# Optimization experiments

Hardware: AMD Instinct MI355X
Metric: run time of the kernel (lower is better)

The kernel has to match this reference:

```python
import jax, jax.numpy as jnp
import numpy as np

B, L, H, V, P = 256, 16, 256, 5000, 4
NPG, DEG, STEPS, OUT = 150, 4, 4, 2000
N, E = B * NPG, B * NPG * DEG


def _seg_softmax(x, seg, num):
    # sparse softmax over variable-size groups (rows of the sparse matrix)
    m = jax.ops.segment_max(x, seg, num_segments=num)
    e = jnp.exp(x - m[seg])
    s = jax.ops.segment_sum(e, seg, num_segments=num)
    return e / s[seg]


def setup_inputs():
    key = jax.random.key(0)
    ks = jax.random.split(key, 24)
    questions = jax.random.normal(ks[0], (B, L, H), jnp.float32)
    lengths = jax.random.randint(ks[1], (B,), L // 2, L + 1)
    node_attrs = jax.random.normal(ks[2], (N, P - 1, H), jnp.float32)
    edge_attrs = jax.random.normal(ks[3], (E, H), jnp.float32)
    node_graph = jnp.repeat(jnp.arange(B), NPG)
    edge_graph = jnp.repeat(jnp.arange(B), NPG * DEG)
    off = jnp.repeat(jnp.arange(B) * NPG, NPG * DEG)
    edge_src = jax.random.randint(ks[4], (E,), 0, NPG) + off
    edge_dst = jax.random.randint(ks[5], (E,), 0, NPG) + off
    s = float(1.0 / np.sqrt(H))
    u = lambda k, shape: jax.random.uniform(k, shape, jnp.float32, -s, s)
    vocab = jax.random.normal(ks[6], (V, H), jnp.float32) * 0.1
    default_embed = jax.random.uniform(ks[7], (H,), jnp.float32)
    W_norm = jnp.eye(H, dtype=jnp.float32)
    lstm_Wih, lstm_Whh = u(ks[8], (4 * H, H)), u(ks[9], (4 * H, H))
    lstm_bih, lstm_bhh = u(ks[10], (4 * H,)), u(ks[11], (4 * H,))
    rnn_Wih, rnn_Whh = u(ks[12], (H, H)), u(ks[13], (H, H))
    rnn_bih, rnn_bhh = u(ks[14], (H,)), u(ks[15], (H,))
    prop_embeds = jax.random.normal(ks[16], (P, H), jnp.float32) * 0.1
    Ws_property = jax.random.uniform(ks[17], (P, H, H), jnp.float32) * s
    W_state = jax.random.uniform(ks[18], (H,), jnp.float32) * s
    W_relation = jax.random.uniform(ks[19], (H,), jnp.float32) * s
    lin_W, lin_b = u(ks[20], (OUT, 2 * H)), u(ks[21], (OUT,))
    return dict(questions=questions, node_attrs=node_attrs, edge_attrs=edge_attrs,
                vocab=vocab, default_embed=default_embed, W_norm=W_norm,
                lstm_Wih=lstm_Wih, lstm_Whh=lstm_Whh, lstm_bih=lstm_bih, lstm_bhh=lstm_bhh,
                rnn_Wih=rnn_Wih, rnn_Whh=rnn_Whh, rnn_bih=rnn_bih, rnn_bhh=rnn_bhh,
                prop_embeds=prop_embeds, Ws_property=Ws_property,
                W_state=W_state, W_relation=W_relation, lin_W=lin_W, lin_b=lin_b,
                lengths=lengths, node_graph=node_graph, edge_graph=edge_graph,
                edge_src=edge_src, edge_dst=edge_dst)


def reference(questions, node_attrs, edge_attrs, vocab, default_embed, W_norm,
              lstm_Wih, lstm_Whh, lstm_bih, lstm_bhh,
              rnn_Wih, rnn_Whh, rnn_bih, rnn_bhh,
              prop_embeds, Ws_property, W_state, W_relation, lin_W, lin_b,
              lengths, node_graph, edge_graph, edge_src, edge_dst):
    # ---- NormalizeWordsModel (tagger) ----
    words = questions.reshape(B * L, H)
    C = jnp.concatenate([vocab, default_embed[None]], axis=0)  # [V+1, H]
    Pm = jax.nn.softmax((words @ W_norm) @ C.T, axis=1)        # [B*L, V+1]
    Vtag = Pm[:, -1:] * words + Pm[:, :-1] @ vocab             # [B*L, H]
    Vpad = Vtag.reshape(B, L, H)

    # ---- LSTM encoder: final hidden at last valid step (packed-sequence semantics) ----
    valid = jnp.arange(L)[:, None] < lengths[None, :]  # [L, B]

    def lstm_step(carry, inp):
        h, c = carry
        x, v = inp
        g = x @ lstm_Wih.T + lstm_bih + h @ lstm_Whh.T + lstm_bhh
        i, f, gc, o = jnp.split(g, 4, axis=-1)  # torch gate order i,f,g,o
        c_new = jax.nn.sigmoid(f) * c + jax.nn.sigmoid(i) * jnp.tanh(gc)
        h_new = jax.nn.sigmoid(o) * jnp.tanh(c_new)
        vm = v[:, None]
        return (jnp.where(vm, h_new, h), jnp.where(vm, c_new, c)), None

    z = jnp.zeros((B, H), questions.dtype)
    (Q, _), _ = jax.lax.scan(lstm_step, (z, z), (Vpad.transpose(1, 0, 2), valid))

    # ---- InstructionsDecoder: relu RNNCell fed the same Q each step ----
    def dec_step(hx, _):
        hx = jax.nn.relu(Q @ rnn_Wih.T + rnn_bih + hx @ rnn_Whh.T + rnn_bhh)
        return hx, hx

    _, Hins = jax.lax.scan(dec_step, z, None, length=STEPS)
    Hins = Hins.transpose(1, 0, 2)  # [B, STEPS, H]

    # ---- attention over (masked) tagged words ----
    att = jnp.einsum('bnh,blh->bnl', Hins, Vpad)
    mask = jnp.arange(L)[None, None, :] < lengths[:, None, None]
    att = jnp.where(mask, att, -jnp.inf)
    R = jax.nn.softmax(att, axis=-1) @ Vpad  # instructions [B, STEPS, H]

    # ---- NSMCell recurrence ----
    nodes_per_graph = jax.ops.segment_sum(jnp.ones(N, questions.dtype), node_graph, num_segments=B)
    dist = (1.0 / nodes_per_graph)[node_graph]  # [N]
    prop_sim = None
    for step in range(STEPS):
        instr = R[:, step]  # [B, H]
        prop_sim = jax.nn.softmax(instr @ prop_embeds.T, axis=1)  # [B, P]
        transformed = jnp.einsum('phk,npk->nph', Ws_property[:-1], node_attrs)  # [N, P-1, H]
        node_scores = jax.nn.elu(jnp.sum(
            prop_sim[node_graph, :-1, None] * instr[node_graph, None, :] * transformed, axis=1))  # [N, H]
        edge_scores = jax.nn.elu(instr[edge_graph] * (edge_attrs @ Ws_property[-1].T))  # [E, H]
        p_state = _seg_softmax(node_scores @ W_state, node_graph, B)  # [N]
        agg = jax.ops.segment_sum(dist[edge_src, None] * edge_scores, edge_dst, num_segments=N)  # [N, H]
        p_rel = _seg_softmax(agg @ W_relation, node_graph, B)  # [N]
        r = prop_sim[node_graph, -1]
        dist = r * p_rel + (1.0 - r) * p_state

    # ---- readout ----
    node_feat = jnp.sum(prop_sim[node_graph, :-1, None] * node_attrs, axis=1)  # [N, H]
    aggregated = jax.ops.segment_sum(dist[:, None] * node_feat, node_graph, num_segments=B)  # [B, H]
    return jnp.concatenate([Q, aggregated], axis=1) @ lin_W.T + lin_b
```

## Files before the change

kernel.cpp:

```cpp
#include <hip/hip_runtime.h>
#include <hip/hip_bf16.h>
#include <math.h>

#define BB 256
#define LL 16
#define HH 256
#define VV 5000
#define NPG 150
#define DEG 4
#define NSTEPS 4
#define OUTD 2000
#define NN (BB*NPG)
#define EE (BB*NPG*DEG)
#define BL (BB*LL)
#define VPAD 5120
#define KPAD 5024
#define EPG (NPG*DEG)

__device__ __forceinline__ float wred_sum(float v){
  #pragma unroll
  for(int o=32;o;o>>=1) v += __shfl_down(v,o,64);
  return v;
}
__device__ __forceinline__ float wred_max(float v){
  #pragma unroll
  for(int o=32;o;o>>=1) v = fmaxf(v,__shfl_down(v,o,64));
  return v;
}
__device__ __forceinline__ float block_sum256(float v, float* sh){
  v = wred_sum(v);
  __syncthreads();
  if((threadIdx.x&63)==0) sh[threadIdx.x>>6]=v;
  __syncthreads();
  return sh[0]+sh[1]+sh[2]+sh[3];
}
__device__ __forceinline__ float block_max256(float v, float* sh){
  v = wred_max(v);
  __syncthreads();
  if((threadIdx.x&63)==0) sh[threadIdx.x>>6]=v;
  __syncthreads();
  return fmaxf(fmaxf(sh[0],sh[1]),fmaxf(sh[2],sh[3]));
}
__device__ __forceinline__ float eluf(float x){ return x>0.f ? x : expm1f(x); }
__device__ __forceinline__ float sigf(float x){ return 1.f/(1.f+expf(-x)); }
__device__ __forceinline__ float fsig(float x){
  return __builtin_amdgcn_rcpf(1.f + __expf(-x));
}
__device__ __forceinline__ float ftanh(float x){
  return 1.f - 2.f*__builtin_amdgcn_rcpf(1.f + __expf(2.f*x));
}
__device__ __forceinline__ float b2f(unsigned short s){
  union{float f; unsigned int u;} x; x.u = ((unsigned int)s)<<16; return x.f;
}
__device__ __forceinline__ unsigned short f2bf_bits(float x){
  union { __hip_bfloat16 h; unsigned short s; } u; u.h = __float2bfloat16(x); return u.s;
}

__device__ __forceinline__ void async16(void* lds, const void* g){
  __builtin_amdgcn_global_load_lds(
      (const __attribute__((address_space(1))) unsigned int*)g,
      (__attribute__((address_space(3))) unsigned int*)lds, 16, 0, 0);
}

typedef __attribute__((ext_vector_type(8))) short short8;
typedef __attribute__((ext_vector_type(4))) float f32x4;

__device__ __forceinline__ short8 pack8(float4 a, float4 b){
  short8 r;
  r[0]=(short)f2bf_bits(a.x); r[1]=(short)f2bf_bits(a.y);
  r[2]=(short)f2bf_bits(a.z); r[3]=(short)f2bf_bits(a.w);
  r[4]=(short)f2bf_bits(b.x); r[5]=(short)f2bf_bits(b.y);
  r[6]=(short)f2bf_bits(b.z); r[7]=(short)f2bf_bits(b.w);
  return r;
}

template<int EPI>
__global__ __launch_bounds__(256) void mfma_bt_bf16_k(
    const __hip_bfloat16* __restrict__ A, const __hip_bfloat16* __restrict__ Bt,
    float* __restrict__ Cf, __hip_bfloat16* __restrict__ Cb,
    int lda, int ldb, int ldc, int Nreal,
    int kItersTotal, int kPerSplit, const float* __restrict__ bias,
    const float* __restrict__ rscale)
{
  __shared__ __hip_bfloat16 As[128*32];
  __shared__ __hip_bfloat16 Bs[128*32];
  const int bm = blockIdx.y*128, bn = blockIdx.x*128;
  const int tid = threadIdx.x;
  int k0 = blockIdx.z * kPerSplit;
  int k1 = k0 + kPerSplit; if (k1 > kItersTotal) k1 = kItersTotal;
  const int lane = tid & 63, wave = tid >> 6;
  const int quad = lane >> 4, r16 = lane & 15;
  const int wr = wave >> 1, wc = wave & 1;
  f32x4 acc[4][4] = {};
  const int c0 = tid, c1 = tid + 256;
  const int ar0 = c0 >> 2, ak0 = (c0 & 3)*8;
  const int ar1 = c1 >> 2, ak1 = (c1 & 3)*8;
  const __hip_bfloat16* Ab = A + (size_t)bm*lda;
  const __hip_bfloat16* Bb = Bt + (size_t)bn*ldb;
  for (int kk = k0; kk < k1; ++kk){
    const int kb = kk*32;
    async16(&As[c0*8], Ab + (size_t)ar0*lda + kb + ak0);
    async16(&As[c1*8], Ab + (size_t)ar1*lda + kb + ak1);
    async16(&Bs[c0*8], Bb + (size_t)ar0*ldb + kb + ak0);
    async16(&Bs[c1*8], Bb + (size_t)ar1*ldb + kb + ak1);
    __syncthreads();
    short8 av[4], bv[4];
    #pragma unroll
    for (int i=0;i<4;i++){
      av[i] = *(const short8*)&As[(wr*64 + i*16 + r16)*32 + quad*8];
      bv[i] = *(const short8*)&Bs[(wc*64 + i*16 + r16)*32 + quad*8];
    }
    #pragma unroll
    for (int i=0;i<4;i++)
      #pragma unroll
      for (int j=0;j<4;j++)
        acc[i][j] = __builtin_amdgcn_mfma_f32_16x16x32_bf16(av[i], bv[j], acc[i][j], 0,0,0);
    __syncthreads();
  }
  #pragma unroll
  for (int i=0;i<4;i++){
    int row = bm + wr*64 + i*16 + quad*4;
    #pragma unroll
    for (int j=0;j<4;j++){
      int col = bn + wc*64 + j*16 + r16;
      if (col >= Nreal) continue;
      #pragma unroll
      for (int r=0;r<4;r++){
        float v = acc[i][j][r];
        if (EPI==0){ if (bias) v += bias[col]; Cf[(size_t)(row+r)*ldc + col] = v; }
        else if (EPI==1){ Cb[(size_t)(row+r)*ldc + col] = __float2bfloat16(v); }
        else { if (rscale) v *= rscale[row+r]; atomicAdd(&Cf[(size_t)(row+r)*ldc + col], v); }
      }
    }
  }
}

template<int EPI>
__global__ __launch_bounds__(256) void mfma_bt_f32_k(
    const float* __restrict__ A, const float* __restrict__ Bt,
    float* __restrict__ Cf, __hip_bfloat16* __restrict__ Cb,
    int lda, int ldb, int ldc, int Nreal,
    int kIters, const float* __restrict__ bias)
{
  __shared__ __hip_bfloat16 As[128*32];
  __shared__ __hip_bfloat16 Bs[128*32];
  const int bm = blockIdx.y*128, bn = blockIdx.x*128;
  const int tid = threadIdx.x;
  const int lane = tid & 63, wave = tid >> 6;
  const int quad = lane >> 4, r16 = lane & 15;
  const int wr = wave >> 1, wc = wave & 1;
  f32x4 acc[4][4] = {};
  for (int kk = 0; kk < kIters; ++kk){
    const int kb = kk*32;
    #pragma unroll
    for (int i=0;i<2;i++){
      int c = tid + i*256;
      int row = c >> 2, k0 = (c & 3)*8;
      const float* src = A + (size_t)(bm+row)*lda + kb + k0;
      float4 v0 = *(const float4*)(src);
      float4 v1 = *(const float4*)(src+4);
      *(short8*)&As[row*32 + k0] = pack8(v0, v1);
    }
    #pragma unroll
    for (int i=0;i<2;i++){
      int c = tid + i*256;
      int row = c >> 2, k0 = (c & 3)*8;
      float4 v0 = {0.f,0.f,0.f,0.f}, v1 = {0.f,0.f,0.f,0.f};
      if (bn + row < Nreal){
        const float* src = Bt + (size_t)(bn+row)*ldb + kb + k0;
        v0 = *(const float4*)(src);
        v1 = *(const float4*)(src+4);
      }
      *(short8*)&Bs[row*32 + k0] = pack8(v0, v1);
    }
    __syncthreads();
    short8 av[4], bv[4];
    #pragma unroll
    for (int i=0;i<4;i++){
      av[i] = *(const short8*)&As[(wr*64 + i*16 + r16)*32 + quad*8];
      bv[i] = *(const short8*)&Bs[(wc*64 + i*16 + r16)*32 + quad*8];
    }
    #pragma unroll
    for (int i=0;i<4;i++)
      #pragma unroll
      for (int j=0;j<4;j++)
        acc[i][j] = __builtin_amdgcn_mfma_f32_16x16x32_bf16(av[i], bv[j], acc[i][j], 0,0,0);
    __syncthreads();
  }
  #pragma unroll
  for (int i=0;i<4;i++){
    int row = bm + wr*64 + i*16 + quad*4;
    #pragma unroll
    for (int j=0;j<4;j++){
      int col = bn + wc*64 + j*16 + r16;
      if (col >= Nreal) continue;
      #pragma unroll
      for (int r=0;r<4;r++){
        float v = acc[i][j][r];
        if (EPI==0){ if (bias) v += bias[col]; Cf[(size_t)(row+r)*ldc + col] = v; }
        else { Cb[(size_t)(row+r)*ldc + col] = __float2bfloat16(v); }
      }
    }
  }
}

__global__ __launch_bounds__(256) void gemm_exp_k(
    const __hip_bfloat16* __restrict__ A, const __hip_bfloat16* __restrict__ Bt,
    __hip_bfloat16* __restrict__ Pm, float* __restrict__ row_sum,
    float* __restrict__ e_def)
{
  __shared__ __hip_bfloat16 As[128*32];
  __shared__ __hip_bfloat16 Bs[128*32];
  const int bm = blockIdx.y*128, bn = blockIdx.x*128;
  const int tid = threadIdx.x;
  const int lane = tid & 63, wave = tid >> 6;
  const int quad = lane >> 4, r16 = lane & 15;
  const int wr = wave >> 1, wc = wave & 1;
  f32x4 acc[4][4] = {};
  const int c0 = tid, c1 = tid + 256;
  const int ar0 = c0 >> 2, ak0 = (c0 & 3)*8;
  const int ar1 = c1 >> 2, ak1 = (c1 & 3)*8;
  const __hip_bfloat16* Ab = A + (size_t)bm*HH;
  const __hip_bfloat16* Bb = Bt + (size_t)bn*HH;
  for (int kk = 0; kk < HH/32; ++kk){
    const int kb = kk*32;
    async16(&As[c0*8], Ab + (size_t)ar0*HH + kb + ak0);
    async16(&As[c1*8], Ab + (size_t)ar1*HH + kb + ak1);
    async16(&Bs[c0*8], Bb + (size_t)ar0*HH + kb + ak0);
    async16(&Bs[c1*8], Bb + (size_t)ar1*HH + kb + ak1);
    __syncthreads();
    short8 av[4], bv[4];
    #pragma unroll
    for (int i=0;i<4;i++){
      av[i] = *(const short8*)&As[(wr*64 + i*16 + r16)*32 + quad*8];
      bv[i] = *(const short8*)&Bs[(wc*64 + i*16 + r16)*32 + quad*8];
    }
    #pragma unroll
    for (int i=0;i<4;i++)
      #pragma unroll
      for (int j=0;j<4;j++)
        acc[i][j] = __builtin_amdgcn_mfma_f32_16x16x32_bf16(av[i], bv[j], acc[i][j], 0,0,0);
    __syncthreads();
  }
  #pragma unroll
  for (int i=0;i<4;i++){
    int rowb = bm + wr*64 + i*16 + quad*4;
    float rsum[4] = {0.f,0.f,0.f,0.f};
    #pragma unroll
    for (int j=0;j<4;j++){
      int col = bn + wc*64 + j*16 + r16;
      #pragma unroll
      for (int r=0;r<4;r++){
        float e = (col <= VV) ? expf(acc[i][j][r]) : 0.f;
        rsum[r] += e;
        if (col < KPAD) Pm[(size_t)(rowb+r)*KPAD + col] = __float2bfloat16(col < VV ? e : 0.f);
        if (col == VV) e_def[rowb+r] = e;
      }
    }
    #pragma unroll
    for (int r=0;r<4;r++){
      float s = rsum[r];
      s += __shfl_xor(s, 1, 64);
      s += __shfl_xor(s, 2, 64);
      s += __shfl_xor(s, 4, 64);
      s += __shfl_xor(s, 8, 64);
      if (r16 == 0) atomicAdd(&row_sum[rowb+r], s);
    }
  }
}

__global__ __launch_bounds__(1024)
__attribute__((amdgpu_waves_per_eu(4, 4)))
void lstm_persist_k(
    const float* __restrict__ gX, const __hip_bfloat16* __restrict__ Whh_bf,
    const int* __restrict__ lengths,
    float* __restrict__ h_out, __hip_bfloat16* __restrict__ hbf_out)
{
  __shared__ __hip_bfloat16 Wl[512*132];
  __shared__ __hip_bfloat16 hbuf[2][16*264];
  const int bg = blockIdx.x, tid = threadIdx.x;
  const int lane = tid & 63, w = tid >> 6;
  const int quad = lane >> 4, r16 = lane & 15;
  const int hb = w*16;
  for (int idx = tid; idx < 512*16; idx += 1024){
    int row = idx >> 4, c8 = (idx & 15)*8;
    int ww = row >> 6, g = (row >> 4) & 3, rr = row & 15;
    *(short8*)&Wl[row*132 + c8] =
        *(const short8*)&Whh_bf[((size_t)(g*256 + ww*16 + rr))*256 + 128 + c8];
  }
  short8 rW[4][4];
  #pragma unroll
  for (int kc=0; kc<4; kc++)
    #pragma unroll
    for (int g=0; g<4; g++)
      rW[kc][g] = *(const short8*)&Whh_bf[((size_t)(g*256 + hb + r16))*256 + kc*32 + quad*8];
  for (int i = tid; i < 16*264; i += 1024) hbuf[0][i] = __float2bfloat16(0.f);
  int lenr[4];
  #pragma unroll
  for (int r=0;r<4;r++) lenr[r] = lengths[bg*16 + quad*4 + r];
  __syncthreads();
  f32x4 cstate = {0.f,0.f,0.f,0.f};
  f32x4 hstate = {0.f,0.f,0.f,0.f};
  int p = 0;
  const float* gXb = gX + (size_t)bg*16*LL*(4*HH) + hb + r16;
  for (int t=0; t<LL; t++){
    float gxv[4][4];
    #pragma unroll
    for (int r=0;r<4;r++)
      #pragma unroll
      for (int g=0;g<4;g++)
        gxv[r][g] = gXb[((size_t)((quad*4+r)*LL + t))*(4*HH) + g*HH];
    f32x4 acc[4] = {};
    const __hip_bfloat16* hr = hbuf[p];
    #pragma unroll
    for (int kc=0; kc<4; kc++){
      short8 a = *(const short8*)&hr[r16*264 + kc*32 + quad*8];
      #pragma unroll
      for (int g=0; g<4; g++)
        acc[g] = __builtin_amdgcn_mfma_f32_16x16x32_bf16(a, rW[kc][g], acc[g], 0,0,0);
    }
    if (w < 8){
      #pragma unroll
      for (int kc=4; kc<8; kc++){
        short8 a = *(const short8*)&hr[r16*264 + kc*32 + quad*8];
        #pragma unroll
        for (int g=0; g<4; g++){
          short8 b = *(const short8*)&Wl[(w*64 + g*16 + r16)*132 + (kc-4)*32 + quad*8];
          acc[g] = __builtin_amdgcn_mfma_f32_16x16x32_bf16(a, b, acc[g], 0,0,0);
        }
      }
    } else {
      #pragma unroll
      for (int kc=4; kc<8; kc++){
        short8 a = *(const short8*)&hr[r16*264 + kc*32 + quad*8];
        #pragma unroll
        for (int g=0; g<4; g++){
          short8 b = *(const short8*)&Whh_bf[((size_t)(g*256 + hb + r16))*256 + kc*32 + quad*8];
          acc[g] = __builtin_amdgcn_mfma_f32_16x16x32_bf16(a, b, acc[g], 0,0,0);
        }
      }
    }
    #pragma unroll
    for (int r=0;r<4;r++){
      int batch = quad*4 + r;
      float gi = acc[0][r] + gxv[r][0];
      float gf = acc[1][r] + gxv[r][1];
      float gc = acc[2][r] + gxv[r][2];
      float go = acc[3][r] + gxv[r][3];
      float cn = fsig(gf)*cstate[r] + fsig(gi)*ftanh(gc);
      float hn = fsig(go)*ftanh(cn);
      if (t < lenr[r]){ cstate[r] = cn; hstate[r] = hn; }
      hbuf[p^1][batch*264 + hb + r16] = __float2bfloat16(hstate[r]);
    }
    p ^= 1;
    __syncthreads();
  }
  #pragma unroll
  for (int r=0;r<4;r++){
    int batch = quad*4 + r;
    size_t o = (size_t)(bg*16+batch)*HH + hb + r16;
    h_out[o] = hstate[r];
    hbf_out[o] = __float2bfloat16(hstate[r]);
  }
}

__global__ __launch_bounds__(1024)
__attribute__((amdgpu_waves_per_eu(4, 4)))
void dec_persist_k(
    const __hip_bfloat16* __restrict__ Qbf, const __hip_bfloat16* __restrict__ Wih_bf,
    const __hip_bfloat16* __restrict__ Whh_bf,
    const float* __restrict__ bih, const float* __restrict__ bhh,
    float* __restrict__ Hins)
{
  __shared__ __hip_bfloat16 Wl[256*264];
  __shared__ __hip_bfloat16 xb[2][16*264];
  const int bg = blockIdx.x, tid = threadIdx.x;
  const int lane = tid & 63, w = tid >> 6;
  const int quad = lane >> 4, r16 = lane & 15;
  const int col = w*16 + r16;
  for (int c = tid; c < 8192; c += 1024){
    int row = c >> 5, ci = (c & 31)*8;
    *(short8*)&Wl[row*264 + ci] = *(const short8*)&Whh_bf[(size_t)row*256 + ci];
  }
  f32x4 qp = {};
  #pragma unroll
  for (int kc=0; kc<8; kc++){
    short8 a = *(const short8*)&Qbf[(size_t)(bg*16 + r16)*HH + kc*32 + quad*8];
    short8 b = *(const short8*)&Wih_bf[(size_t)col*HH + kc*32 + quad*8];
    qp = __builtin_amdgcn_mfma_f32_16x16x32_bf16(a, b, qp, 0,0,0);
  }
  const float bihv = bih[col], bhhv = bhh[col];
  __syncthreads();
  #pragma unroll
  for (int r=0;r<4;r++){
    int batch = quad*4 + r;
    float v = fmaxf(qp[r] + bihv + bhhv, 0.f);
    xb[0][batch*264 + col] = __float2bfloat16(v);
    Hins[(size_t)(bg*16+batch)*(NSTEPS*HH) + 0*HH + col] = v;
  }
  __syncthreads();
  int p = 0;
  for (int s=1; s<NSTEPS; s++){
    f32x4 acc = {};
    #pragma unroll
    for (int kc=0; kc<8; kc++){
      short8 a = *(const short8*)&xb[p][r16*264 + kc*32 + quad*8];
      short8 b = *(const short8*)&Wl[col*264 + kc*32 + quad*8];
      acc = __builtin_amdgcn_mfma_f32_16x16x32_bf16(a, b, acc, 0,0,0);
    }
    #pragma unroll
    for (int r=0;r<4;r++){
      int batch = quad*4 + r;
      float v = fmaxf(qp[r] + bihv + acc[r] + bhhv, 0.f);
      xb[p^1][batch*264 + col] = __float2bfloat16(v);
      Hins[(size_t)(bg*16+batch)*(NSTEPS*HH) + s*HH + col] = v;
    }
    p ^= 1;
    __syncthreads();
  }
}

__global__ void cvt_bf16_k(const float* __restrict__ src, __hip_bfloat16* __restrict__ dst, int n){
  int i = (blockIdx.x*256 + threadIdx.x)*4;
  if (i >= n) return;
  float4 v = *(const float4*)(src + i);
  dst[i]   = __float2bfloat16(v.x);
  dst[i+1] = __float2bfloat16(v.y);
  dst[i+2] = __float2bfloat16(v.z);
  dst[i+3] = __float2bfloat16(v.w);
}

__global__ void tr_cvt_k(const float* __restrict__ src, __hip_bfloat16* __restrict__ dst, int R, int Ccols){
  int idx = blockIdx.x*256 + threadIdx.x;
  if (idx >= R*Ccols) return;
  int r = idx / Ccols, c = idx % Ccols;
  dst[(size_t)c*R + r] = __float2bfloat16(src[idx]);
}

__global__ void build_cb_k(const float* __restrict__ vocab, const float* __restrict__ de,
                           __hip_bfloat16* __restrict__ Cb){
  int idx = blockIdx.x*256 + threadIdx.x;
  if (idx >= VPAD*HH) return;
  int v = idx >> 8, h = idx & 255;
  float x = (v < VV) ? vocab[(size_t)v*HH + h] : (v == VV ? de[h] : 0.f);
  Cb[idx] = __float2bfloat16(x);
}

__global__ void build_vt_k(const float* __restrict__ vocab, __hip_bfloat16* __restrict__ VT){
  int idx = blockIdx.x*256 + threadIdx.x;
  if (idx >= HH*KPAD) return;
  int h = idx / KPAD, v = idx % KPAD;
  VT[idx] = __float2bfloat16(v < VV ? vocab[(size_t)v*HH + h] : 0.f);
}

__global__ void bsum_k(const float* a, const float* b, float* o){
  int i = blockIdx.x*256 + threadIdx.x;
  if (i < 4*HH) o[i] = a[i] + b[i];
}

__global__ void zero_k(float* p, int n){
  int idx = blockIdx.x*256 + threadIdx.x;
  if (idx < n) p[idx] = 0.f;
}

__global__ void inv_k(float* p, int n){
  int idx = blockIdx.x*256 + threadIdx.x;
  if (idx < n) p[idx] = 1.f/p[idx];
}

__global__ void vtag_epi_k(float* __restrict__ Vtag, const float* __restrict__ e_def,
                           const float* __restrict__ inv_s, const float* __restrict__ words){
  int r = blockIdx.x, h = threadIdx.x;
  size_t o = (size_t)r*HH + h;
  Vtag[o] += e_def[r]*inv_s[r]*words[o];
}

__global__ __launch_bounds__(256) void attention_k(const float* __restrict__ Vtag,
                                                   const float* __restrict__ Hins,
                                                   const int* __restrict__ lengths,
                                                   float* __restrict__ R){
  __shared__ float Vl[LL][HH];
  __shared__ float Hn[NSTEPS][HH];
  __shared__ float att[NSTEPS][LL];
  int b = blockIdx.x, tid = threadIdx.x;
  for (int idx=tid; idx<LL*HH; idx+=256){ int l=idx>>8, h=idx&255; Vl[l][h] = Vtag[((size_t)b*LL+l)*HH + h]; }
  for (int idx=tid; idx<NSTEPS*HH; idx+=256){ Hn[idx>>8][idx&255] = Hins[(size_t)b*(NSTEPS*HH) + idx]; }
  __syncthreads();
  if (tid < NSTEPS*LL){
    int n2 = tid>>4, l = tid&15;
    float s = 0.f;
    for (int k=0;k<HH;k++) s += Hn[n2][k]*Vl[l][k];
    att[n2][l] = s;
  }
  __syncthreads();
  int len = lengths[b];
  if (tid < NSTEPS){
    float m = -1e30f;
    for (int l=0;l<len;l++) m = fmaxf(m, att[tid][l]);
    float s = 0.f;
    for (int l=0;l<LL;l++){ float e = (l<len)? expf(att[tid][l]-m) : 0.f; att[tid][l]=e; s+=e; }
    float inv = 1.f/s;
    for (int l=0;l<LL;l++) att[tid][l] *= inv;
  }
  __syncthreads();
  {
    int n2 = tid>>6, h0 = (tid&63)*4;
    float r0=0,r1=0,r2=0,r3=0;
    for (int l=0;l<LL;l++){
      float w = att[n2][l];
      r0 += w*Vl[l][h0]; r1 += w*Vl[l][h0+1]; r2 += w*Vl[l][h0+2]; r3 += w*Vl[l][h0+3];
    }
    float* o = R + (size_t)b*(NSTEPS*HH) + n2*HH + h0;
    o[0]=r0; o[1]=r1; o[2]=r2; o[3]=r3;
  }
}

__global__ __launch_bounds__(256) void prop_sim_all_k(const float* __restrict__ R,
                                                      const float* __restrict__ pe,
                                                      float* __restrict__ psa){
  __shared__ float sp[4];
  int gb = blockIdx.x;
  int s = gb >> 8, b = gb & 255;
  int tid = threadIdx.x;
  int p = tid>>6, lane = tid&63;
  const float* instr = R + (size_t)b*(NSTEPS*HH) + s*HH;
  float v = 0.f;
  for (int h=lane; h<HH; h+=64) v += instr[h]*pe[p*HH+h];
  v = wred_sum(v);
  if (lane==0) sp[p] = v;
  __syncthreads();
  if (tid==0){
    float m = fmaxf(fmaxf(sp[0],sp[1]),fmaxf(sp[2],sp[3]));
    float e0=expf(sp[0]-m), e1=expf(sp[1]-m), e2=expf(sp[2]-m), e3=expf(sp[3]-m);
    float ss = e0+e1+e2+e3;
    float* o = psa + (size_t)s*BB*4 + b*4;
    o[0]=e0/ss; o[1]=e1/ss; o[2]=e2/ss; o[3]=e3/ss;
  }
}

__global__ __launch_bounds__(256) void nsm_all_k(
    const __hip_bfloat16* __restrict__ Tf, const __hip_bfloat16* __restrict__ ET,
    const float* __restrict__ R, const float* __restrict__ psa,
    const float* __restrict__ W_state, const float* __restrict__ Wr,
    float* __restrict__ s_state_all, float* __restrict__ acc_e_all)
{
  const int wave = threadIdx.x >> 6, lane = threadIdx.x & 63;
  const int h0 = lane*4;
  if (blockIdx.x < NN/4){
    int n = blockIdx.x*4 + wave;
    int g = n / NPG;
    const unsigned short* t = (const unsigned short*)(Tf + (size_t)n*(3*HH));
    ushort4 t0 = *(const ushort4*)(t + h0);
    ushort4 t1 = *(const ushort4*)(t + HH + h0);
    ushort4 t2 = *(const ushort4*)(t + 2*HH + h0);
    float4 wv = *(const float4*)(W_state + h0);
    #pragma unroll
    for (int s=0; s<NSTEPS; s++){
      const float* instr = R + (size_t)g*(NSTEPS*HH) + s*HH;
      const float* ps = psa + (size_t)s*BB*4 + g*4;
      float ps0 = ps[0], ps1 = ps[1], ps2 = ps[2];
      float4 iv = *(const float4*)(instr + h0);
      float acc;
      acc  = eluf(iv.x*(ps0*b2f(t0.x)+ps1*b2f(t1.x)+ps2*b2f(t2.x)))*wv.x;
      acc += eluf(iv.y*(ps0*b2f(t0.y)+ps1*b2f(t1.y)+ps2*b2f(t2.y)))*wv.y;
      acc += eluf(iv.z*(ps0*b2f(t0.z)+ps1*b2f(t1.z)+ps2*b2f(t2.z)))*wv.z;
      acc += eluf(iv.w*(ps0*b2f(t0.w)+ps1*b2f(t1.w)+ps2*b2f(t2.w)))*wv.w;
      acc = wred_sum(acc);
      if (lane==0) s_state_all[(size_t)s*NN + n] = acc;
    }
  } else {
    int e = (blockIdx.x - NN/4)*4 + wave;
    int b = e / (NPG*DEG);
    const unsigned short* et = (const unsigned short*)(ET + (size_t)e*HH);
    ushort4 ev = *(const ushort4*)(et + h0);
    float4 wv = *(const float4*)(Wr + h0);
    #pragma unroll
    for (int s=0; s<NSTEPS; s++){
      const float* instr = R + (size_t)b*(NSTEPS*HH) + s*HH;
      float4 iv = *(const float4*)(instr + h0);
      float acc;
      acc  = eluf(iv.x*b2f(ev.x))*wv.x;
      acc += eluf(iv.y*b2f(ev.y))*wv.y;
      acc += eluf(iv.z*b2f(ev.z))*wv.z;
      acc += eluf(iv.w*b2f(ev.w))*wv.w;
      acc = wred_sum(acc);
      if (lane==0) acc_e_all[(size_t)s*EE + e] = acc;
    }
  }
}

__global__ __launch_bounds__(256) void nsm_steps_k(
    const float* __restrict__ s_state_all, const float* __restrict__ acc_e_all,
    const int* __restrict__ esrc, const int* __restrict__ edst,
    const float* __restrict__ psa, float* __restrict__ dist_out)
{
  __shared__ float nd[NPG];
  __shared__ float srel[NPG];
  __shared__ float sh[4];
  __shared__ short les[EPG], led[EPG];
  const int b = blockIdx.x, tid = threadIdx.x;
  const int base_e = b*EPG, base_n = b*NPG;
  for (int j = tid; j < EPG; j += 256){
    les[j] = (short)(esrc[base_e + j] - base_n);
    led[j] = (short)(edst[base_e + j] - base_n);
  }
  if (tid < NPG){ nd[tid] = 1.f/(float)NPG; srel[tid] = 0.f; }
  __syncthreads();
  for (int s=0; s<NSTEPS; s++){
    for (int j = tid; j < EPG; j += 256){
      float v = nd[les[j]] * acc_e_all[(size_t)s*EE + base_e + j];
      atomicAdd(&srel[led[j]], v);
    }
    __syncthreads();
    bool ok = (tid < NPG);
    float ss = ok ? s_state_all[(size_t)s*NN + base_n + tid] : -1e30f;
    float sr = ok ? srel[tid] : -1e30f;
    float m1 = block_max256(ss, sh);
    float e1 = ok ? expf(ss - m1) : 0.f;
    float d1 = block_sum256(e1, sh);
    float m2 = block_max256(sr, sh);
    float e2 = ok ? expf(sr - m2) : 0.f;
    float d2 = block_sum256(e2, sh);
    __syncthreads();
    if (ok){
      float r = psa[(size_t)s*BB*4 + b*4 + 3];
      nd[tid] = r*(e2/d2) + (1.f-r)*(e1/d1);
      srel[tid] = 0.f;
    }
    __syncthreads();
  }
  if (tid < NPG) dist_out[base_n + tid] = nd[tid];
}

__global__ __launch_bounds__(256) void final_agg_k(const float* __restrict__ na, const float* __restrict__ dist,
                                                   const float* __restrict__ ps, float* __restrict__ aggregated){
  int b = blockIdx.x, h = threadIdx.x;
  float ps0 = ps[b*4+0], ps1 = ps[b*4+1], ps2 = ps[b*4+2];
  float acc = 0.f;
  for (int i=0;i<NPG;i++){
    int n = b*NPG + i;
    float d = dist[n];
    const float* a = na + (size_t)n*(3*HH);
    acc += d*(ps0*a[h] + ps1*a[HH+h] + ps2*a[2*HH+h]);
  }
  aggregated[b*HH + h] = acc;
}

__global__ void qa_build_k(const float* __restrict__ Q, const float* __restrict__ aggregated,
                           float* __restrict__ QA){
  int idx = blockIdx.x*256 + threadIdx.x;
  if (idx >= BB*2*HH) return;
  int b = idx >> 9, k = idx & 511;
  QA[idx] = (k < HH) ? Q[b*HH + k] : aggregated[b*HH + (k-HH)];
}

extern "C" void kernel_launch(void* const* d_in, const int* in_sizes, int n_in,
                              void* d_out, int out_size, void* d_ws, size_t ws_size,
                              hipStream_t stream) {
  (void)in_sizes; (void)n_in; (void)out_size; (void)ws_size;
  const float* questions     = (const float*)d_in[0];
  const float* node_attrs    = (const float*)d_in[1];
  const float* edge_attrs    = (const float*)d_in[2];
  const float* vocab         = (const float*)d_in[3];
  const float* default_embed = (const float*)d_in[4];
  const float* W_norm        = (const float*)d_in[5];
  const float* lstm_Wih      = (const float*)d_in[6];
  const float* lstm_Whh      = (const float*)d_in[7];
  const float* lstm_bih      = (const float*)d_in[8];
  const float* lstm_bhh      = (const float*)d_in[9];
  const float* rnn_Wih       = (const float*)d_in[10];
  const float* rnn_Whh       = (const float*)d_in[11];
  const float* rnn_bih       = (const float*)d_in[12];
  const float* rnn_bhh       = (const float*)d_in[13];
  const float* prop_embeds   = (const float*)d_in[14];
  const float* Ws_property   = (const float*)d_in[15];
  const float* W_state       = (const float*)d_in[16];
  const float* W_relation    = (const float*)d_in[17];
  const float* lin_W         = (const float*)d_in[18];
  const float* lin_b         = (const float*)d_in[19];
  const int*   lengths       = (const int*)d_in[20];
  const int*   edge_src      = (const int*)d_in[23];
  const int*   edge_dst      = (const int*)d_in[24];
  float* out = (float*)d_out;

  char* base = (char*)d_ws;
  size_t off = 0;
  auto alloc = [&](size_t nbytes)->void*{
    void* p = base + off;
    off += (nbytes + 255) & ~(size_t)255;
    return p;
  };

  __hip_bfloat16* qbf     = (__hip_bfloat16*)alloc((size_t)BL*HH*2);
  __hip_bfloat16* WnT_bf  = (__hip_bfloat16*)alloc((size_t)HH*HH*2);
  __hip_bfloat16* xw_bf   = (__hip_bfloat16*)alloc((size_t)BL*HH*2);
  __hip_bfloat16* Cbv     = (__hip_bfloat16*)alloc((size_t)VPAD*HH*2);
  __hip_bfloat16* vT_bf   = (__hip_bfloat16*)alloc((size_t)HH*KPAD*2);
  __hip_bfloat16* Whh_bf  = (__hip_bfloat16*)alloc((size_t)4*HH*HH*2);
  __hip_bfloat16* rWih_bf = (__hip_bfloat16*)alloc((size_t)HH*HH*2);
  __hip_bfloat16* rWhh_bf = (__hip_bfloat16*)alloc((size_t)HH*HH*2);
  __hip_bfloat16* h_bf    = (__hip_bfloat16*)alloc((size_t)BB*HH*2);
  float* e_def    = (float*)alloc((size_t)BL*4);
  float* row_sum  = (float*)alloc((size_t)BL*4);
  float* Vtag     = (float*)alloc((size_t)BL*HH*4);
  float* bsum     = (float*)alloc((size_t)4*HH*4);
  float* h_buf    = (float*)alloc((size_t)BB*HH*4);
  float* Hins     = (float*)alloc((size_t)BB*NSTEPS*HH*4);
  float* R        = (float*)alloc((size_t)BB*NSTEPS*HH*4);
  float* psa      = (float*)alloc((size_t)NSTEPS*BB*4*4);
  float* s_state_all = (float*)alloc((size_t)NSTEPS*NN*4);
  float* acc_e_all   = (float*)alloc((size_t)NSTEPS*EE*4);
  float* dist     = (float*)alloc((size_t)NN*4);
  float* aggregated = (float*)alloc((size_t)BB*HH*4);
  float* QA       = (float*)alloc((size_t)BB*2*HH*4);
  __hip_bfloat16* Pm_bf = (__hip_bfloat16*)alloc((size_t)BL*KPAD*2);
  char*  TfR      = (char*)alloc((size_t)NN*3*HH*2);
  __hip_bfloat16* Tf = (__hip_bfloat16*)TfR;
  float* gX          = (float*)TfR;
  __hip_bfloat16* ET = (__hip_bfloat16*)alloc((size_t)EE*HH*2);

  cvt_bf16_k<<<(BL*HH/4+255)/256, 256, 0, stream>>>(questions, qbf, BL*HH);
  tr_cvt_k<<<(HH*HH+255)/256, 256, 0, stream>>>(W_norm, WnT_bf, HH, HH);
  build_cb_k<<<(VPAD*HH+255)/256, 256, 0, stream>>>(vocab, default_embed, Cbv);
  build_vt_k<<<(HH*KPAD+255)/256, 256, 0, stream>>>(vocab, vT_bf);
  cvt_bf16_k<<<(4*HH*HH/4+255)/256, 256, 0, stream>>>(lstm_Whh, Whh_bf, 4*HH*HH);
  cvt_bf16_k<<<(HH*HH/4+255)/256, 256, 0, stream>>>(rnn_Wih, rWih_bf, HH*HH);
  cvt_bf16_k<<<(HH*HH/4+255)/256, 256, 0, stream>>>(rnn_Whh, rWhh_bf, HH*HH);
  bsum_k<<<(4*HH+255)/256, 256, 0, stream>>>(lstm_bih, lstm_bhh, bsum);
  zero_k<<<(BL+255)/256, 256, 0, stream>>>(row_sum, BL);
  zero_k<<<(BL*HH+255)/256, 256, 0, stream>>>(Vtag, BL*HH);

  mfma_bt_bf16_k<1><<<dim3(2,32,1), 256, 0, stream>>>(qbf, WnT_bf, nullptr, xw_bf,
      HH, HH, HH, HH, HH/32, HH/32, nullptr, nullptr);
  gemm_exp_k<<<dim3(VPAD/128, BL/128, 1), 256, 0, stream>>>(xw_bf, Cbv, Pm_bf, row_sum, e_def);
  inv_k<<<(BL+255)/256, 256, 0, stream>>>(row_sum, BL);
  mfma_bt_bf16_k<2><<<dim3(HH/128, BL/128, 8), 256, 0, stream>>>(
      Pm_bf, vT_bf, Vtag, nullptr, KPAD, KPAD, HH, HH, KPAD/32, 20, nullptr, row_sum);
  vtag_epi_k<<<BL, HH, 0, stream>>>(Vtag, e_def, row_sum, questions);

  mfma_bt_f32_k<0><<<dim3(8,32,1), 256, 0, stream>>>(Vtag, lstm_Wih, gX, nullptr,
      HH, HH, 4*HH, 4*HH, HH/32, bsum);
  lstm_persist_k<<<16, 1024, 0, stream>>>(gX, Whh_bf, lengths, h_buf, h_bf);

  dec_persist_k<<<16, 1024, 0, stream>>>(h_bf, rWih_bf, rWhh_bf, rnn_bih, rnn_bhh, Hins);

  attention_k<<<BB, 256, 0, stream>>>(Vtag, Hins, lengths, R);
  prop_sim_all_k<<<NSTEPS*BB, 256, 0, stream>>>(R, prop_embeds, psa);

  for (int p=0; p<3; p++)
    mfma_bt_f32_k<1><<<dim3(2,NN/128,1), 256, 0, stream>>>(
        node_attrs + (size_t)p*HH, Ws_property + (size_t)p*HH*HH,
        nullptr, Tf + (size_t)p*HH, 3*HH, HH, 3*HH, HH, HH/32, nullptr);
  mfma_bt_f32_k<1><<<dim3(2,EE/128,1), 256, 0, stream>>>(
      edge_attrs, Ws_property + (size_t)3*HH*HH,
      nullptr, ET, HH, HH, HH, HH, HH/32, nullptr);

  nsm_all_k<<<NN/4 + EE/4, 256, 0, stream>>>(
      Tf, ET, R, psa, W_state, W_relation, s_state_all, acc_e_all);
  nsm_steps_k<<<BB, 256, 0, stream>>>(
      s_state_all, acc_e_all, edge_src, edge_dst, psa, dist);

  final_agg_k<<<BB, 256, 0, stream>>>(node_attrs, dist, psa + (size_t)3*BB*4, aggregated);
  qa_build_k<<<(BB*2*HH+255)/256, 256, 0, stream>>>(h_buf, aggregated, QA);
  mfma_bt_f32_k<0><<<dim3(16,2,1), 256, 0, stream>>>(QA, lin_W, out, nullptr,
      2*HH, 2*HH, OUTD, OUTD, 2*HH/32, lin_b);
}
```

Measured before the change: 983.4 us.

## Fuse edge projection GEMM with per-step edge score epilogue

```diff
diff --git a/kernel.cpp b/kernel.cpp
--- a/kernel.cpp
+++ b/kernel.cpp
@@ -64,6 +64,8 @@
 
 typedef __attribute__((ext_vector_type(8))) short short8;
 typedef __attribute__((ext_vector_type(4))) float f32x4;
+
+#define KEEPV(x) asm volatile("" : "+v"(x))
 
 __device__ __forceinline__ short8 pack8(float4 a, float4 b){
   short8 r;
@@ -292,8 +294,10 @@
   #pragma unroll
   for (int kc=0; kc<4; kc++)
     #pragma unroll
-    for (int g=0; g<4; g++)
+    for (int g=0; g<4; g++){
       rW[kc][g] = *(const short8*)&Whh_bf[((size_t)(g*256 + hb + r16))*256 + kc*32 + quad*8];
+      KEEPV(rW[kc][g]);
+    }
   for (int i = tid; i < 16*264; i += 1024) hbuf[0][i] = __float2bfloat16(0.f);
   int lenr[4];
   #pragma unroll
@@ -538,53 +542,124 @@
   }
 }
 
-__global__ __launch_bounds__(256) void nsm_all_k(
-    const __hip_bfloat16* __restrict__ Tf, const __hip_bfloat16* __restrict__ ET,
+__global__ __launch_bounds__(256) void nsm_node_k(
+    const __hip_bfloat16* __restrict__ Tf,
     const float* __restrict__ R, const float* __restrict__ psa,
-    const float* __restrict__ W_state, const float* __restrict__ Wr,
-    float* __restrict__ s_state_all, float* __restrict__ acc_e_all)
+    const float* __restrict__ W_state,
+    float* __restrict__ s_state_all)
 {
   const int wave = threadIdx.x >> 6, lane = threadIdx.x & 63;
   const int h0 = lane*4;
-  if (blockIdx.x < NN/4){
-    int n = blockIdx.x*4 + wave;
-    int g = n / NPG;
-    const unsigned short* t = (const unsigned short*)(Tf + (size_t)n*(3*HH));
-    ushort4 t0 = *(const ushort4*)(t + h0);
-    ushort4 t1 = *(const ushort4*)(t + HH + h0);
-    ushort4 t2 = *(const ushort4*)(t + 2*HH + h0);
-    float4 wv = *(const float4*)(W_state + h0);
-    #pragma unroll
-    for (int s=0; s<NSTEPS; s++){
-      const float* instr = R + (size_t)g*(NSTEPS*HH) + s*HH;
-      const float* ps = psa + (size_t)s*BB*4 + g*4;
-      float ps0 = ps[0], ps1 = ps[1], ps2 = ps[2];
-      float4 iv = *(const float4*)(instr + h0);
-      float acc;
-      acc  = eluf(iv.x*(ps0*b2f(t0.x)+ps1*b2f(t1.x)+ps2*b2f(t2.x)))*wv.x;
-      acc += eluf(iv.y*(ps0*b2f(t0.y)+ps1*b2f(t1.y)+ps2*b2f(t2.y)))*wv.y;
-      acc += eluf(iv.z*(ps0*b2f(t0.z)+ps1*b2f(t1.z)+ps2*b2f(t2.z)))*wv.z;
-      acc += eluf(iv.w*(ps0*b2f(t0.w)+ps1*b2f(t1.w)+ps2*b2f(t2.w)))*wv.w;
-      acc = wred_sum(acc);
-      if (lane==0) s_state_all[(size_t)s*NN + n] = acc;
-    }
-  } else {
-    int e = (blockIdx.x - NN/4)*4 + wave;
-    int b = e / (NPG*DEG);
-    const unsigned short* et = (const unsigned short*)(ET + (size_t)e*HH);
-    ushort4 ev = *(const ushort4*)(et + h0);
-    float4 wv = *(const float4*)(Wr + h0);
-    #pragma unroll
-    for (int s=0; s<NSTEPS; s++){
-      const float* instr = R + (size_t)b*(NSTEPS*HH) + s*HH;
-      float4 iv = *(const float4*)(instr + h0);
-      float acc;
-      acc  = eluf(iv.x*b2f(ev.x))*wv.x;
-      acc += eluf(iv.y*b2f(ev.y))*wv.y;
-      acc += eluf(iv.z*b2f(ev.z))*wv.z;
-      acc += eluf(iv.w*b2f(ev.w))*wv.w;
-      acc = wred_sum(acc);
-      if (lane==0) acc_e_all[(size_t)s*EE + e] = acc;
+  int n = blockIdx.x*4 + wave;
+  int g = n / NPG;
+  const unsigned short* t = (const unsigned short*)(Tf + (size_t)n*(3*HH));
+  ushort4 t0 = *(const ushort4*)(t + h0);
+  ushort4 t1 = *(const ushort4*)(t + HH + h0);
+  ushort4 t2 = *(const ushort4*)(t + 2*HH + h0);
+  float4 wv = *(const float4*)(W_state + h0);
+  #pragma unroll
+  for (int s=0; s<NSTEPS; s++){
+    const float* instr = R + (size_t)g*(NSTEPS*HH) + s*HH;
+    const float* ps = psa + (size_t)s*BB*4 + g*4;
+    float ps0 = ps[0], ps1 = ps[1], ps2 = ps[2];
+    float4 iv = *(const float4*)(instr + h0);
+    float acc;
+    acc  = eluf(iv.x*(ps0*b2f(t0.x)+ps1*b2f(t1.x)+ps2*b2f(t2.x)))*wv.x;
+    acc += eluf(iv.y*(ps0*b2f(t0.y)+ps1*b2f(t1.y)+ps2*b2f(t2.y)))*wv.y;
+    acc += eluf(iv.z*(ps0*b2f(t0.z)+ps1*b2f(t1.z)+ps2*b2f(t2.z)))*wv.z;
+    acc += eluf(iv.w*(ps0*b2f(t0.w)+ps1*b2f(t1.w)+ps2*b2f(t2.w)))*wv.w;
+    acc = wred_sum(acc);
+    if (lane==0) s_state_all[(size_t)s*NN + n] = acc;
+  }
+}
+
+__global__ __launch_bounds__(256) void edge_gemm_score_k(
+    const float* __restrict__ A,
+    const float* __restrict__ Bt,
+    const float* __restrict__ R,
+    const float* __restrict__ Wr,
+    float* __restrict__ acc_e_all)
+{
+  __shared__ __hip_bfloat16 As[128*32];
+  __shared__ __hip_bfloat16 Bs[256*32];
+  __shared__ float Rl[2][NSTEPS][HH];
+  __shared__ float wrl[HH];
+  const int bm = blockIdx.x*128;
+  const int tid = threadIdx.x;
+  const int lane = tid & 63, wave = tid >> 6;
+  const int quad = lane >> 4, r16 = lane & 15;
+  const int g0 = bm / EPG;
+  const int g1 = (bm + 127) / EPG;
+  for (int idx = tid; idx < 2*NSTEPS*HH; idx += 256){
+    int gg = idx >> 10, rem = idx & 1023;
+    int g = gg ? g1 : g0;
+    Rl[gg][rem >> 8][rem & 255] = R[(size_t)g*(NSTEPS*HH) + rem];
+  }
+  for (int idx = tid; idx < HH; idx += 256) wrl[idx] = Wr[idx];
+  f32x4 acc[2][16] = {};
+  for (int kk = 0; kk < HH/32; ++kk){
+    const int kb = kk*32;
+    #pragma unroll
+    for (int i=0;i<2;i++){
+      int c = tid + i*256;
+      int row = c >> 2, k0 = (c & 3)*8;
+      const float* src = A + (size_t)(bm+row)*HH + kb + k0;
+      float4 v0 = *(const float4*)(src);
+      float4 v1 = *(const float4*)(src+4);
+      *(short8*)&As[row*32 + k0] = pack8(v0, v1);
+    }
+    #pragma unroll
+    for (int i=0;i<4;i++){
+      int c = tid + i*256;
+      int row = c >> 2, k0 = (c & 3)*8;
+      const float* src = Bt + (size_t)row*HH + kb + k0;
+      float4 v0 = *(const float4*)(src);
+      float4 v1 = *(const float4*)(src+4);
+      *(short8*)&Bs[row*32 + k0] = pack8(v0, v1);
+    }
+    __syncthreads();
+    short8 av[2];
+    #pragma unroll
+    for (int i=0;i<2;i++)
+      av[i] = *(const short8*)&As[(wave*32 + i*16 + r16)*32 + quad*8];
+    #pragma unroll
+    for (int j=0;j<16;j++){
+      short8 bv = *(const short8*)&Bs[(j*16 + r16)*32 + quad*8];
+      acc[0][j] = __builtin_amdgcn_mfma_f32_16x16x32_bf16(av[0], bv, acc[0][j], 0,0,0);
+      acc[1][j] = __builtin_amdgcn_mfma_f32_16x16x32_bf16(av[1], bv, acc[1][j], 0,0,0);
+    }
+    __syncthreads();
+  }
+  #pragma unroll
+  for (int i=0;i<2;i++){
+    #pragma unroll
+    for (int r=0;r<4;r++){
+      int e = bm + wave*32 + i*16 + quad*4 + r;
+      int gsel = (e/EPG != g0) ? 1 : 0;
+      float s0=0.f, s1=0.f, s2=0.f, s3=0.f;
+      #pragma unroll
+      for (int j=0;j<16;j++){
+        int col = j*16 + r16;
+        float c = acc[i][j][r];
+        float w = wrl[col];
+        s0 += eluf(Rl[gsel][0][col]*c)*w;
+        s1 += eluf(Rl[gsel][1][col]*c)*w;
+        s2 += eluf(Rl[gsel][2][col]*c)*w;
+        s3 += eluf(Rl[gsel][3][col]*c)*w;
+      }
+      #pragma unroll
+      for (int m=1; m<16; m<<=1){
+        s0 += __shfl_xor(s0, m, 64);
+        s1 += __shfl_xor(s1, m, 64);
+        s2 += __shfl_xor(s2, m, 64);
+        s3 += __shfl_xor(s3, m, 64);
+      }
+      if (r16 == 0){
+        acc_e_all[(size_t)0*EE + e] = s0;
+        acc_e_all[(size_t)1*EE + e] = s1;
+        acc_e_all[(size_t)2*EE + e] = s2;
+        acc_e_all[(size_t)3*EE + e] = s3;
+      }
     }
   }
 }
@@ -717,7 +792,6 @@
   char*  TfR      = (char*)alloc((size_t)NN*3*HH*2);
   __hip_bfloat16* Tf = (__hip_bfloat16*)TfR;
   float* gX          = (float*)TfR;
-  __hip_bfloat16* ET = (__hip_bfloat16*)alloc((size_t)EE*HH*2);
 
   cvt_bf16_k<<<(BL*HH/4+255)/256, 256, 0, stream>>>(questions, qbf, BL*HH);
   tr_cvt_k<<<(HH*HH+255)/256, 256, 0, stream>>>(W_norm, WnT_bf, HH, HH);
@@ -751,12 +825,10 @@
     mfma_bt_f32_k<1><<<dim3(2,NN/128,1), 256, 0, stream>>>(
         node_attrs + (size_t)p*HH, Ws_property + (size_t)p*HH*HH,
         nullptr, Tf + (size_t)p*HH, 3*HH, HH, 3*HH, HH, HH/32, nullptr);
-  mfma_bt_f32_k<1><<<dim3(2,EE/128,1), 256, 0, stream>>>(
-      edge_attrs, Ws_property + (size_t)3*HH*HH,
-      nullptr, ET, HH, HH, HH, HH, HH/32, nullptr);
-
-  nsm_all_k<<<NN/4 + EE/4, 256, 0, stream>>>(
-      Tf, ET, R, psa, W_state, W_relation, s_state_all, acc_e_all);
+  edge_gemm_score_k<<<EE/128, 256, 0, stream>>>(
+      edge_attrs, Ws_property + (size_t)3*HH*HH, R, W_relation, acc_e_all);
+
+  nsm_node_k<<<NN/4, 256, 0, stream>>>(Tf, R, psa, W_state, s_state_all);
   nsm_steps_k<<<BB, 256, 0, stream>>>(
       s_state_all, acc_e_all, edge_src, edge_dst, psa, dist);
 
```

Result: slower. 1.517 ms (+54.3%).
